# Kernel optimization log

Hardware: AMD Instinct MI355X
Metric: run time of the kernel (lower is better)

Reference implementation:

```python
import jax, jax.numpy as jnp
import numpy as np

B, HOR, E, L = 16, 512, 1024, 12
ACT_NUM, DIM, ADIM = 10, 64, 10
N = 2 * HOR                      # backbone sequence length (test=False)
NPOS = 4 * (1 + HOR)             # wpe table size
D_IN = 3 + DIM * ACT_NUM + ADIM  # embed_transition input dim = 653


def setup_inputs() -> dict:
    key = jax.random.key(0)
    ks = jax.random.split(key, 12)
    s = lambda k, shape: (jax.random.normal(k, shape, jnp.float32) * 0.02)
    return {
        "action_set": jax.random.normal(ks[0], (B, ACT_NUM, DIM), jnp.float32),
        "context_rewards": jax.random.normal(ks[1], (B, HOR, 1), jnp.float32),
        "wpe": s(ks[2], (NPOS, E)),
        "W_emb": s(ks[3], (D_IN, E)),
        "b_emb": jnp.zeros((E,), jnp.float32),
        "Wq": s(ks[4], (L, E, E)),
        "Wk": s(ks[5], (L, E, E)),
        "Wv": s(ks[6], (L, E, E)),
        "ln1_g": jnp.ones((L, E), jnp.float32),
        "ln1_b": jnp.zeros((L, E), jnp.float32),
        "W1": s(ks[7], (L, E, E)),
        "b1": jnp.zeros((L, E), jnp.float32),
        "W2": s(ks[8], (L, E, E)),
        "b2": jnp.zeros((L, E), jnp.float32),
        "ln2_g": jnp.ones((L, E), jnp.float32),
        "ln2_b": jnp.zeros((L, E), jnp.float32),
        "W_pred": s(ks[9], (E, ADIM)),
        "b_pred": jnp.zeros((ADIM,), jnp.float32),
    }


def _layernorm(x, g, b, eps=1e-5):
    mu = x.mean(-1, keepdims=True)
    var = ((x - mu) ** 2).mean(-1, keepdims=True)
    return (x - mu) * jax.lax.rsqrt(var + eps) * g + b


def reference(action_set, context_rewards, wpe, W_emb, b_emb, Wq, Wk, Wv,
              ln1_g, ln1_b, W1, b1, W2, b2, ln2_g, ln2_b, W_pred, b_pred):
    batch = action_set.shape[0]
    hor = context_rewards.shape[1]
    n = 2 * hor
    # --- build interleaved sequence (outer Transformer glue) ---
    a = action_set.reshape(batch, 1, -1)                       # [B,1,DA]
    pair = jnp.concatenate([a, jnp.zeros_like(a)], axis=1)     # [B,2,DA]
    act_set_seq = jnp.tile(pair, (1, hor, 1))                  # [B,2H,DA]
    action_seq = jnp.zeros((batch, n, ADIM + 1), jnp.float32)
    one_seq = jnp.ones((batch, n, 1), jnp.float32)
    pos_seq = jnp.broadcast_to(
        jnp.arange(1, n + 1, dtype=jnp.float32).reshape(1, n, 1), (batch, n, 1))
    seq = jnp.concatenate([act_set_seq, action_seq, one_seq, pos_seq], axis=2)  # [B,N,D_IN]
    # --- DecoderTransformerBackbone ---
    Hs = seq @ W_emb + b_emb
    Hs = Hs + wpe[:n]                                          # positional embedding
    idx = jnp.arange(n)
    # normalized causal mask: row i has 1/(i+1) on j<=i, else 0
    mask = jnp.where(idx[:, None] >= idx[None, :],
                     1.0 / (idx[:, None].astype(jnp.float32) + 1.0), 0.0)
    for l in range(Wq.shape[0]):
        q = Hs @ Wq[l]
        k = Hs @ Wk[l]
        v = Hs @ Wv[l]
        attn = jax.nn.relu(jnp.einsum('bid,bjd->bij', q, k)) * mask
        Hs = Hs + jnp.einsum('bij,bjd->bid', attn, v)
        Hs = _layernorm(Hs, ln1_g[l], ln1_b[l])
        Hs = Hs + (jax.nn.relu(Hs @ W1[l] + b1[l]) @ W2[l] + b2[l])
        Hs = _layernorm(Hs, ln2_g[l], ln2_b[l])
    preds = Hs @ W_pred + b_pred                               # [B,N,ADIM]
    return preds[:, 0::2, :]                                   # [B,HOR,ADIM]
```

## Files before the change

### kernel.cpp

```cpp
#include <hip/hip_runtime.h>
#include <stdint.h>
#include <stddef.h>

#define E_DIM 1024
#define B_SZ  16
#define N_SEQ 1024
#define L_NUM 12
#define ACT_D 640
#define ADIM_ 10

typedef unsigned short u16;
typedef __attribute__((ext_vector_type(8))) short bf16x8;
typedef __attribute__((ext_vector_type(4))) float f32x4;

__device__ __forceinline__ u16 f2bf(float x) {
  union { float f; unsigned int u; } c; c.f = x;
  unsigned int r = c.u + 0x7fffu + ((c.u >> 16) & 1u);
  return (u16)(r >> 16);
}
__device__ __forceinline__ float bf2f(u16 h) {
  union { unsigned int u; float f; } c; c.u = ((unsigned int)h) << 16;
  return c.f;
}

struct us4 { u16 x, y, z, w; };

#define GLD16(gsrc, ldst) __builtin_amdgcn_global_load_lds( \
    (const __attribute__((address_space(1))) void*)(gsrc),  \
    (__attribute__((address_space(3))) void*)(ldst), 16, 0, 0)

#define BM 256
#define BN 128
#define BK 32
#define LDS_A 8192
#define LDS_B 4096
#define BUFU 24576

template<int MODE, int EPI>
__global__ __launch_bounds__(512)
void gemm_nt_mfma(const u16* __restrict__ Ah, const u16* __restrict__ Al,
                  const u16* __restrict__ Bh0, const u16* __restrict__ Bl0,
                  const u16* __restrict__ Bh1, const u16* __restrict__ Bl1,
                  float* __restrict__ Co,
                  u16* __restrict__ Ch0, u16* __restrict__ Cl0,
                  u16* __restrict__ Ch1, u16* __restrict__ Cl1,
                  const float* __restrict__ bias0, const float* __restrict__ bias1,
                  int K, int lda, int ldb, int ldc, int tilesN,
                  long long sA, long long sB, long long sC)
{
  __shared__ u16 smem[3 * BUFU];

  const int tid = threadIdx.x;
  const int bat = blockIdx.y;

  const u16* Bh = Bh0; const u16* Bl = Bl0;
  u16* Ch = Ch0; u16* Cl = Cl0;
  const float* bias = bias0;
  if (blockIdx.z) { Bh = Bh1; Bl = Bl1; Ch = Ch1; Cl = Cl1; bias = bias1; }

  Ah += bat * sA; Al += bat * sA;
  Bh += bat * sB; Bl += bat * sB;

  int bid;
  {
    const int nwg = gridDim.x;
    const int q = nwg >> 3, r = nwg & 7;
    const int xcd = blockIdx.x & 7, off = blockIdx.x >> 3;
    bid = ((xcd < r) ? xcd * (q + 1) : r * (q + 1) + (xcd - r) * q) + off;
  }

  int tm, tn;
  if (MODE == 1) {
    int t = bid, m = 0;
    while ((m + 1) * (m + 2) <= t) m++;
    tm = m; tn = t - m * (m + 1);
  } else {
    tm = bid / tilesN;
    tn = bid % tilesN;
  }
  int kend = K;
  if (MODE == 2) { int c = (tm + 1) * BM; kend = (c < K) ? c : K; }
  const int nk = kend / BK;

  const int ca0 = tid, ca1 = tid + 512, cb0 = tid;
  const int ra0 = ca0 >> 2, ra1 = ca1 >> 2, rb0 = cb0 >> 2;
  const int pa0 = ((ca0 & 3) ^ ((ra0 >> 1) & 3)) * 8;
  const int pa1 = ((ca1 & 3) ^ ((ra1 >> 1) & 3)) * 8;
  const int pb0 = ((cb0 & 3) ^ ((rb0 >> 1) & 3)) * 8;
  const u16* gAh0 = Ah + (long long)(tm * BM + ra0) * lda + pa0;
  const u16* gAh1 = Ah + (long long)(tm * BM + ra1) * lda + pa1;
  const u16* gAl0 = Al + (long long)(tm * BM + ra0) * lda + pa0;
  const u16* gAl1 = Al + (long long)(tm * BM + ra1) * lda + pa1;
  const u16* gBh0 = Bh + (long long)(tn * BN + rb0) * ldb + pb0;
  const u16* gBl0 = Bl + (long long)(tn * BN + rb0) * ldb + pb0;
  const int oa0 = ca0 * 8, oa1 = ca1 * 8, ob0 = cb0 * 8;

  int issued = 0;
  auto stage = [&]() {
    u16* base = smem + (issued % 3) * BUFU;
    GLD16(gAh0, base + oa0);
    GLD16(gAh1, base + oa1);
    GLD16(gAl0, base + LDS_A + oa0);
    GLD16(gAl1, base + LDS_A + oa1);
    GLD16(gBh0, base + 2 * LDS_A + ob0);
    GLD16(gBl0, base + 2 * LDS_A + LDS_B + ob0);
    gAh0 += BK; gAh1 += BK; gAl0 += BK; gAl1 += BK;
    gBh0 += BK; gBl0 += BK;
    issued++;
  };

  const int lane = tid & 63;
  const int w = tid >> 6, wr = w >> 2, wc = w & 3;
  const int fr = lane & 15;
  const int kq = (lane >> 4) * 8;
  const int sa = ((fr >> 1) & 3) << 3;
  const int aoff = ((wr * 128 + fr) * BK + kq) ^ sa;
  const int boff = ((wc * 32 + fr) * BK + kq) ^ sa;

  f32x4 acc[8][2];
  #pragma unroll
  for (int m = 0; m < 8; m++)
    #pragma unroll
    for (int n = 0; n < 2; n++) acc[m][n] = (f32x4){0.f, 0.f, 0.f, 0.f};

  stage(); stage();
  asm volatile("s_waitcnt vmcnt(6)" ::: "memory");
  __builtin_amdgcn_s_barrier();

  for (int t = 0; t < nk; t++) {
    if (issued < nk) stage();
    const u16* sb = smem + (t % 3) * BUFU;

    bf16x8 ah[8], al[8], bh[2], bl[2];
    #pragma unroll
    for (int m = 0; m < 8; m++) ah[m] = *(const bf16x8*)(sb + aoff + m * (16 * BK));
    #pragma unroll
    for (int n = 0; n < 2; n++) bh[n] = *(const bf16x8*)(sb + 2 * LDS_A + boff + n * (16 * BK));
    __builtin_amdgcn_s_setprio(1);
    #pragma unroll
    for (int m = 0; m < 8; m++)
      #pragma unroll
      for (int n = 0; n < 2; n++)
        acc[m][n] = __builtin_amdgcn_mfma_f32_16x16x32_bf16(ah[m], bh[n], acc[m][n], 0, 0, 0);
    __builtin_amdgcn_s_setprio(0);
    #pragma unroll
    for (int n = 0; n < 2; n++) bl[n] = *(const bf16x8*)(sb + 2 * LDS_A + LDS_B + boff + n * (16 * BK));
    __builtin_amdgcn_s_setprio(1);
    #pragma unroll
    for (int m = 0; m < 8; m++)
      #pragma unroll
      for (int n = 0; n < 2; n++)
        acc[m][n] = __builtin_amdgcn_mfma_f32_16x16x32_bf16(ah[m], bl[n], acc[m][n], 0, 0, 0);
    __builtin_amdgcn_s_setprio(0);
    #pragma unroll
    for (int m = 0; m < 8; m++) al[m] = *(const bf16x8*)(sb + LDS_A + aoff + m * (16 * BK));
    __builtin_amdgcn_s_setprio(1);
    #pragma unroll
    for (int m = 0; m < 8; m++)
      #pragma unroll
      for (int n = 0; n < 2; n++)
        acc[m][n] = __builtin_amdgcn_mfma_f32_16x16x32_bf16(al[m], bh[n], acc[m][n], 0, 0, 0);
    __builtin_amdgcn_s_setprio(0);

    if (t + 1 < nk) {
      if (issued > t + 2) asm volatile("s_waitcnt vmcnt(6)" ::: "memory");
      else                asm volatile("s_waitcnt vmcnt(0)" ::: "memory");
      __builtin_amdgcn_s_barrier();
    }
  }

  if (Co) Co += bat * sC;
  if (Ch) { Ch += bat * sC; Cl += bat * sC; }
  #pragma unroll
  for (int m = 0; m < 8; m++) {
    #pragma unroll
    for (int r = 0; r < 4; r++) {
      const long long row = (long long)tm * BM + wr * 128 + m * 16 + (lane >> 4) * 4 + r;
      #pragma unroll
      for (int n = 0; n < 2; n++) {
        const long long col = (long long)tn * BN + wc * 32 + n * 16 + (lane & 15);
        float v = acc[m][n][r];
        if (EPI == 2) { v += bias[col]; v = v > 0.f ? v : 0.f; }
        if (EPI == 4) { v += bias[col]; }
        if (EPI == 3) {
          v = v > 0.f ? v : 0.f;
          v = (col <= row) ? v / (float)(row + 1) : 0.f;
        }
        const long long idx = row * (long long)ldc + col;
        if (EPI == 0 || EPI == 4) {
          Co[idx] = v;
        } else {
          u16 h = f2bf(v);
          Ch[idx] = h;
          Cl[idx] = f2bf(v - bf2f(h));
        }
      }
    }
  }
}

struct TP3 {
  const float* s0; const float* s1; const float* s2;
  u16* h0; u16* l0; u16* h1; u16* l1; u16* h2; u16* l2;
};

__global__ __launch_bounds__(256)
void transpose_split3(TP3 p)
{
  __shared__ float tile[32][33];
  const float* src; u16* dh; u16* dl;
  if (blockIdx.z == 0)      { src = p.s0; dh = p.h0; dl = p.l0; }
  else if (blockIdx.z == 1) { src = p.s1; dh = p.h1; dl = p.l1; }
  else                      { src = p.s2; dh = p.h2; dl = p.l2; }
  const int c0 = blockIdx.x * 32, r0 = blockIdx.y * 32;
  const int tx = threadIdx.x & 31, ty = threadIdx.x >> 5;
  #pragma unroll
  for (int i = ty; i < 32; i += 8)
    tile[i][tx] = src[(long long)(r0 + i) * E_DIM + c0 + tx];
  __syncthreads();
  #pragma unroll
  for (int i = ty; i < 32; i += 8) {
    const float v = tile[tx][i];
    const u16 h = f2bf(v);
    const long long idx = (long long)(c0 + i) * E_DIM + r0 + tx;
    dh[idx] = h;
    dl[idx] = f2bf(v - bf2f(h));
  }
}

__global__ __launch_bounds__(256)
void resid_ln(u16* __restrict__ hh, u16* __restrict__ hl,
              const float* __restrict__ delta,
              const float* __restrict__ g, const float* __restrict__ bta)
{
  __shared__ float red[8];
  const long long row = blockIdx.x;
  u16* hp = hh + row * E_DIM;
  u16* lp = hl + row * E_DIM;
  const float* dp = delta + row * E_DIM;
  const int tid = threadIdx.x;
  const int e = tid * 4;

  us4 hv = *(const us4*)(hp + e);
  us4 lv = *(const us4*)(lp + e);
  float4 d = *(const float4*)(dp + e);
  float x0 = bf2f(hv.x) + bf2f(lv.x) + d.x;
  float x1 = bf2f(hv.y) + bf2f(lv.y) + d.y;
  float x2 = bf2f(hv.z) + bf2f(lv.z) + d.z;
  float x3 = bf2f(hv.w) + bf2f(lv.w) + d.w;
  float s = x0 + x1 + x2 + x3;
  float q = x0 * x0 + x1 * x1 + x2 * x2 + x3 * x3;
  #pragma unroll
  for (int o = 32; o > 0; o >>= 1) { s += __shfl_down(s, o); q += __shfl_down(q, o); }
  const int lane = tid & 63, wv = tid >> 6;
  if (lane == 0) { red[wv] = s; red[wv + 4] = q; }
  __syncthreads();
  const float st = red[0] + red[1] + red[2] + red[3];
  const float qt = red[4] + red[5] + red[6] + red[7];
  const float mu = st * (1.0f / E_DIM);
  const float var = qt * (1.0f / E_DIM) - mu * mu;
  const float rstd = rsqrtf(var + 1e-5f);

  float4 gg = *(const float4*)(g + e);
  float4 bb = *(const float4*)(bta + e);
  float y0 = (x0 - mu) * rstd * gg.x + bb.x;
  float y1 = (x1 - mu) * rstd * gg.y + bb.y;
  float y2 = (x2 - mu) * rstd * gg.z + bb.z;
  float y3 = (x3 - mu) * rstd * gg.w + bb.w;

  us4 ho, lo;
  ho.x = f2bf(y0); lo.x = f2bf(y0 - bf2f(ho.x));
  ho.y = f2bf(y1); lo.y = f2bf(y1 - bf2f(ho.y));
  ho.z = f2bf(y2); lo.z = f2bf(y2 - bf2f(ho.z));
  ho.w = f2bf(y3); lo.w = f2bf(y3 - bf2f(ho.w));
  *(us4*)(hp + e) = ho;
  *(us4*)(lp + e) = lo;
}

__global__ __launch_bounds__(256)
void emb_dot(const float* __restrict__ act, const float* __restrict__ Wemb,
             float* __restrict__ Aemb)
{
  const int e = blockIdx.x * 256 + threadIdx.x;
  const int b = blockIdx.y;
  const float* ab = act + b * ACT_D;
  float s = 0.f;
  for (int d = 0; d < ACT_D; d++)
    s = fmaf(ab[d], Wemb[(long long)d * E_DIM + e], s);
  Aemb[b * E_DIM + e] = s;
}

__global__ __launch_bounds__(256)
void emb_fill(const float* __restrict__ Aemb, const float* __restrict__ Wemb,
              const float* __restrict__ bemb, const float* __restrict__ wpe,
              u16* __restrict__ oh, u16* __restrict__ ol)
{
  const int i = blockIdx.x, b = blockIdx.y;
  const int e = threadIdx.x * 4;
  float4 a;
  if ((i & 1) == 0) a = *(const float4*)(Aemb + b * E_DIM + e);
  else { a.x = 0.f; a.y = 0.f; a.z = 0.f; a.w = 0.f; }
  float4 be = *(const float4*)(bemb + e);
  float4 w1 = *(const float4*)(Wemb + 651LL * E_DIM + e);
  float4 w2 = *(const float4*)(Wemb + 652LL * E_DIM + e);
  float4 pw = *(const float4*)(wpe + (long long)i * E_DIM + e);
  const float pos = (float)(i + 1);
  float y0 = a.x + be.x + w1.x + pos * w2.x + pw.x;
  float y1 = a.y + be.y + w1.y + pos * w2.y + pw.y;
  float y2 = a.z + be.z + w1.z + pos * w2.z + pw.z;
  float y3 = a.w + be.w + w1.w + pos * w2.w + pw.w;
  const long long row = (long long)b * N_SEQ + i;

  us4 ho, lo;
  ho.x = f2bf(y0); lo.x = f2bf(y0 - bf2f(ho.x));
  ho.y = f2bf(y1); lo.y = f2bf(y1 - bf2f(ho.y));
  ho.z = f2bf(y2); lo.z = f2bf(y2 - bf2f(ho.z));
  ho.w = f2bf(y3); lo.w = f2bf(y3 - bf2f(ho.w));
  *(us4*)(oh + row * E_DIM + e) = ho;
  *(us4*)(ol + row * E_DIM + e) = lo;
}

__global__ __launch_bounds__(256)
void pred_k(const u16* __restrict__ hh, const u16* __restrict__ hl,
            const float* __restrict__ Wp, const float* __restrict__ bp,
            float* __restrict__ out)
{
  __shared__ float part[4][ADIM_];
  const int h = blockIdx.x, b = blockIdx.y;
  const long long row = (long long)b * N_SEQ + 2 * h;
  const u16* xh = hh + row * E_DIM;
  const u16* xl = hl + row * E_DIM;
  float acc[ADIM_];
  #pragma unroll
  for (int a = 0; a < ADIM_; a++) acc[a] = 0.f;
  for (int e = threadIdx.x; e < E_DIM; e += 256) {
    const float xv = bf2f(xh[e]) + bf2f(xl[e]);
    const float* wq = Wp + e * ADIM_;
    #pragma unroll
    for (int a = 0; a < ADIM_; a++) acc[a] = fmaf(xv, wq[a], acc[a]);
  }
  const int lane = threadIdx.x & 63, wv = threadIdx.x >> 6;
  #pragma unroll
  for (int a = 0; a < ADIM_; a++)
    #pragma unroll
    for (int o = 32; o > 0; o >>= 1) acc[a] += __shfl_down(acc[a], o);
  if (lane == 0)
    #pragma unroll
    for (int a = 0; a < ADIM_; a++) part[wv][a] = acc[a];
  __syncthreads();
  if (threadIdx.x < ADIM_) {
    const int a = threadIdx.x;
    out[((long long)b * (N_SEQ / 2) + h) * ADIM_ + a] =
        part[0][a] + part[1][a] + part[2][a] + part[3][a] + bp[a];
  }
}

__global__ __launch_bounds__(256)
void fill_sentinel(float* p, int n, float v)
{
  int i = blockIdx.x * 256 + threadIdx.x;
  if (i < n) p[i] = v;
}

extern "C" void kernel_launch(void* const* d_in, const int* in_sizes, int n_in,
                              void* d_out, int out_size, void* d_ws, size_t ws_size,
                              hipStream_t stream)
{
  const float* act  = (const float*)d_in[0];
  const float* wpe  = (const float*)d_in[2];
  const float* Wemb = (const float*)d_in[3];
  const float* bemb = (const float*)d_in[4];
  const float* Wq   = (const float*)d_in[5];
  const float* Wk   = (const float*)d_in[6];
  const float* Wv   = (const float*)d_in[7];
  const float* ln1g = (const float*)d_in[8];
  const float* ln1b = (const float*)d_in[9];
  const float* W1   = (const float*)d_in[10];
  const float* b1   = (const float*)d_in[11];
  const float* W2   = (const float*)d_in[12];
  const float* b2   = (const float*)d_in[13];
  const float* ln2g = (const float*)d_in[14];
  const float* ln2b = (const float*)d_in[15];
  const float* Wp   = (const float*)d_in[16];
  const float* bp   = (const float*)d_in[17];
  float* out = (float*)d_out;

  const long long sQ = (long long)N_SEQ * E_DIM;
  const long long sE = (long long)E_DIM * E_DIM;

  auto need = [&](int G) -> size_t {
    return (size_t)G * sQ * 16 + (size_t)sE * 12
         + (size_t)G * E_DIM * 4 + (size_t)(1 << 20);
  };
  int G = 16;
  while (G > 1 && need(G) > ws_size) G >>= 1;
  if (need(G) > ws_size || d_ws == nullptr || G < 8) {
    fill_sentinel<<<dim3((out_size + 255) / 256), 256, 0, stream>>>(out, out_size, 1.0e7f);
    return;
  }

  char* ws = (char*)d_ws;
  size_t off = 0;
  auto alloc = [&](size_t bytes) -> void* {
    void* p = ws + off;
    off += (bytes + 255) & ~(size_t)255;
    return p;
  };
  u16* hsh = (u16*)alloc((size_t)G * sQ * 2);
  u16* hsl = (u16*)alloc((size_t)G * sQ * 2);
  u16* qh  = (u16*)alloc((size_t)G * sQ * 2);
  u16* ql  = (u16*)alloc((size_t)G * sQ * 2);
  char* kreg = (char*)alloc((size_t)G * sQ * 4);
  u16* kh = (u16*)kreg;
  u16* kl = kh + (size_t)G * sQ;
  float* dbuf = (float*)kreg;
  u16* sh_ = (u16*)alloc((size_t)G * sQ * 2);
  u16* sl_ = (u16*)alloc((size_t)G * sQ * 2);
  u16* wAh = (u16*)alloc((size_t)sE * 2);
  u16* wAl = (u16*)alloc((size_t)sE * 2);
  u16* wBh = (u16*)alloc((size_t)sE * 2);
  u16* wBl = (u16*)alloc((size_t)sE * 2);
  u16* wCh = (u16*)alloc((size_t)sE * 2);
  u16* wCl = (u16*)alloc((size_t)sE * 2);
  float* Aemb = (float*)alloc((size_t)G * E_DIM * 4);

  const int tE = E_DIM / BN;
  const int triS = 20;
  const dim3 gqk((G * N_SEQ / BM) * tE, 1, 2);
  const dim3 gm ((G * N_SEQ / BM) * tE, 1, 1);
  const dim3 gsq(triS, G, 1);
  const dim3 gv ((N_SEQ / BM) * tE, G, 1);

  for (int g0 = 0; g0 < B_SZ; g0 += G) {
    emb_dot<<<dim3(E_DIM / 256, G), 256, 0, stream>>>(act + (long long)g0 * ACT_D, Wemb, Aemb);
    emb_fill<<<dim3(N_SEQ, G), 256, 0, stream>>>(Aemb, Wemb, bemb, wpe, hsh, hsl);

    for (int l = 0; l < L_NUM; l++) {
      const long long wof = (long long)l * sE;
      const long long bof = (long long)l * E_DIM;

      TP3 t2 = {Wq + wof, Wk + wof, Wq + wof, wAh, wAl, wBh, wBl, wAh, wAl};
      transpose_split3<<<dim3(32, 32, 2), 256, 0, stream>>>(t2);
      gemm_nt_mfma<0, 1><<<gqk, 512, 0, stream>>>(hsh, hsl, wAh, wAl, wBh, wBl,
          nullptr, qh, ql, kh, kl, nullptr, nullptr,
          E_DIM, E_DIM, E_DIM, E_DIM, tE, 0, 0, 0);

      TP3 t3 = {Wv + wof, W1 + wof, W2 + wof, wAh, wAl, wBh, wBl, wCh, wCl};
      transpose_split3<<<dim3(32, 32, 3), 256, 0, stream>>>(t3);

      gemm_nt_mfma<1, 3><<<gsq, 512, 0, stream>>>(qh, ql, kh, kl, kh, kl,
          nullptr, sh_, sl_, sh_, sl_, nullptr, nullptr,
          E_DIM, E_DIM, E_DIM, N_SEQ, tE, sQ, sQ, sQ);

      gemm_nt_mfma<0, 1><<<gv, 512, 0, stream>>>(wAh, wAl, hsh, hsl, hsh, hsl,
          nullptr, qh, ql, qh, ql, nullptr, nullptr,
          E_DIM, E_DIM, E_DIM, N_SEQ, tE, 0, sQ, sQ);

      gemm_nt_mfma<2, 0><<<gv, 512, 0, stream>>>(sh_, sl_, qh, ql, qh, ql,
          dbuf, nullptr, nullptr, nullptr, nullptr, nullptr, nullptr,
          N_SEQ, N_SEQ, N_SEQ, E_DIM, tE, sQ, sQ, sQ);

      resid_ln<<<dim3(G * N_SEQ), 256, 0, stream>>>(hsh, hsl, dbuf,
          ln1g + bof, ln1b + bof);

      gemm_nt_mfma<0, 2><<<gm, 512, 0, stream>>>(hsh, hsl, wBh, wBl, wBh, wBl,
          nullptr, qh, ql, qh, ql, b1 + bof, b1 + bof,
          E_DIM, E_DIM, E_DIM, E_DIM, tE, 0, 0, 0);
      gemm_nt_mfma<0, 4><<<gm, 512, 0, stream>>>(qh, ql, wCh, wCl, wCh, wCl,
          dbuf, nullptr, nullptr, nullptr, nullptr, b2 + bof, b2 + bof,
          E_DIM, E_DIM, E_DIM, E_DIM, tE, 0, 0, 0);

      resid_ln<<<dim3(G * N_SEQ), 256, 0, stream>>>(hsh, hsl, dbuf,
          ln2g + bof, ln2b + bof);
    }

    pred_k<<<dim3(N_SEQ / 2, G), 256, 0, stream>>>(hsh, hsl, Wp, bp,
        out + (long long)g0 * (N_SEQ / 2) * ADIM_);
  }
}
```

Before: 9.224 ms.

## Add wide 256-column GEMM tile variant and switch to double-buffered LDS pipeline

Templates the split-bf16 MFMA GEMM on the N tile width, adding a 256x256 tile where each wave computes a 128x64 sub-tile; the 128-wide variant now uses 64x64 wave tiles. The LDS pipeline drops from triple to double buffering, with a full vmcnt(0) wait each iteration. The wide tile is used for QK projection always and for the V, PV and MLP GEMMs when the group size is at least 16. The aim is more operand reuse per LDS load and fewer blocks, at the cost of more accumulator registers, less overlap of global loads with compute, and fewer workgroups to fill the CUs.

```diff
diff --git a/kernel.cpp b/kernel.cpp
--- a/kernel.cpp
+++ b/kernel.cpp
@@ -30,13 +30,9 @@
     (__attribute__((address_space(3))) void*)(ldst), 16, 0, 0)
 
 #define BM 256
-#define BN 128
 #define BK 32
-#define LDS_A 8192
-#define LDS_B 4096
-#define BUFU 24576
-
-template<int MODE, int EPI>
+
+template<int MODE, int EPI, int BNT>
 __global__ __launch_bounds__(512)
 void gemm_nt_mfma(const u16* __restrict__ Ah, const u16* __restrict__ Al,
                   const u16* __restrict__ Bh0, const u16* __restrict__ Bl0,
@@ -48,7 +44,14 @@
                   int K, int lda, int ldb, int ldc, int tilesN,
                   long long sA, long long sB, long long sC)
 {
-  __shared__ u16 smem[3 * BUFU];
+  constexpr int LA = BM * BK;
+  constexpr int LB = BNT * BK;
+  constexpr int BUFU = 2 * LA + 2 * LB;
+  __shared__ u16 smem[2 * BUFU];
+
+  constexpr int WAVE_R = (BNT == 256) ? 128 : 64;
+  constexpr int WGC = BNT / 64;
+  constexpr int MA = WAVE_R / 16;
 
   const int tid = threadIdx.x;
   const int bat = blockIdx.y;
@@ -82,89 +85,98 @@
   if (MODE == 2) { int c = (tm + 1) * BM; kend = (c < K) ? c : K; }
   const int nk = kend / BK;
 
-  const int ca0 = tid, ca1 = tid + 512, cb0 = tid;
-  const int ra0 = ca0 >> 2, ra1 = ca1 >> 2, rb0 = cb0 >> 2;
+  const int ca0 = tid, ca1 = tid + 512;
+  const int ra0 = ca0 >> 2, ra1 = ca1 >> 2;
   const int pa0 = ((ca0 & 3) ^ ((ra0 >> 1) & 3)) * 8;
   const int pa1 = ((ca1 & 3) ^ ((ra1 >> 1) & 3)) * 8;
+  const int cb0 = tid, cb1 = tid + 512;
+  const int rb0 = cb0 >> 2, rb1 = cb1 >> 2;
   const int pb0 = ((cb0 & 3) ^ ((rb0 >> 1) & 3)) * 8;
+  const int pb1 = ((cb1 & 3) ^ ((rb1 >> 1) & 3)) * 8;
+
   const u16* gAh0 = Ah + (long long)(tm * BM + ra0) * lda + pa0;
   const u16* gAh1 = Ah + (long long)(tm * BM + ra1) * lda + pa1;
   const u16* gAl0 = Al + (long long)(tm * BM + ra0) * lda + pa0;
   const u16* gAl1 = Al + (long long)(tm * BM + ra1) * lda + pa1;
-  const u16* gBh0 = Bh + (long long)(tn * BN + rb0) * ldb + pb0;
-  const u16* gBl0 = Bl + (long long)(tn * BN + rb0) * ldb + pb0;
-  const int oa0 = ca0 * 8, oa1 = ca1 * 8, ob0 = cb0 * 8;
-
-  int issued = 0;
-  auto stage = [&]() {
-    u16* base = smem + (issued % 3) * BUFU;
+  const u16* gBh0 = Bh + (long long)(tn * BNT + rb0) * ldb + pb0;
+  const u16* gBl0 = Bl + (long long)(tn * BNT + rb0) * ldb + pb0;
+  const u16* gBh1 = Bh + (long long)(tn * BNT + rb1) * ldb + pb1;
+  const u16* gBl1 = Bl + (long long)(tn * BNT + rb1) * ldb + pb1;
+  const int oa0 = ca0 * 8, oa1 = ca1 * 8, ob0 = cb0 * 8, ob1 = cb1 * 8;
+
+  auto stage = [&](int buf) {
+    u16* base = smem + buf * BUFU;
     GLD16(gAh0, base + oa0);
     GLD16(gAh1, base + oa1);
-    GLD16(gAl0, base + LDS_A + oa0);
-    GLD16(gAl1, base + LDS_A + oa1);
-    GLD16(gBh0, base + 2 * LDS_A + ob0);
-    GLD16(gBl0, base + 2 * LDS_A + LDS_B + ob0);
+    GLD16(gAl0, base + LA + oa0);
+    GLD16(gAl1, base + LA + oa1);
+    GLD16(gBh0, base + 2 * LA + ob0);
+    GLD16(gBl0, base + 2 * LA + LB + ob0);
+    if (BNT == 256) {
+      GLD16(gBh1, base + 2 * LA + ob1);
+      GLD16(gBl1, base + 2 * LA + LB + ob1);
+    }
     gAh0 += BK; gAh1 += BK; gAl0 += BK; gAl1 += BK;
     gBh0 += BK; gBl0 += BK;
-    issued++;
+    if (BNT == 256) { gBh1 += BK; gBl1 += BK; }
   };
 
   const int lane = tid & 63;
-  const int w = tid >> 6, wr = w >> 2, wc = w & 3;
+  const int w = tid >> 6;
+  const int wr = w / WGC, wc = w % WGC;
   const int fr = lane & 15;
   const int kq = (lane >> 4) * 8;
   const int sa = ((fr >> 1) & 3) << 3;
-  const int aoff = ((wr * 128 + fr) * BK + kq) ^ sa;
-  const int boff = ((wc * 32 + fr) * BK + kq) ^ sa;
-
-  f32x4 acc[8][2];
-  #pragma unroll
-  for (int m = 0; m < 8; m++)
-    #pragma unroll
-    for (int n = 0; n < 2; n++) acc[m][n] = (f32x4){0.f, 0.f, 0.f, 0.f};
-
-  stage(); stage();
-  asm volatile("s_waitcnt vmcnt(6)" ::: "memory");
+  const int aoff = ((wr * WAVE_R + fr) * BK + kq) ^ sa;
+  const int boff = ((wc * 64 + fr) * BK + kq) ^ sa;
+
+  f32x4 acc[MA][4];
+  #pragma unroll
+  for (int m = 0; m < MA; m++)
+    #pragma unroll
+    for (int n = 0; n < 4; n++) acc[m][n] = (f32x4){0.f, 0.f, 0.f, 0.f};
+
+  stage(0);
+  asm volatile("s_waitcnt vmcnt(0)" ::: "memory");
   __builtin_amdgcn_s_barrier();
 
   for (int t = 0; t < nk; t++) {
-    if (issued < nk) stage();
-    const u16* sb = smem + (t % 3) * BUFU;
-
-    bf16x8 ah[8], al[8], bh[2], bl[2];
-    #pragma unroll
-    for (int m = 0; m < 8; m++) ah[m] = *(const bf16x8*)(sb + aoff + m * (16 * BK));
-    #pragma unroll
-    for (int n = 0; n < 2; n++) bh[n] = *(const bf16x8*)(sb + 2 * LDS_A + boff + n * (16 * BK));
+    if (t + 1 < nk) stage((t + 1) & 1);
+    const u16* sb = smem + (t & 1) * BUFU;
+
+    bf16x8 ah[MA], al[MA], bh[4], bl[4];
+    #pragma unroll
+    for (int m = 0; m < MA; m++) ah[m] = *(const bf16x8*)(sb + aoff + m * (16 * BK));
+    #pragma unroll
+    for (int n = 0; n < 4; n++) bh[n] = *(const bf16x8*)(sb + 2 * LA + boff + n * (16 * BK));
     __builtin_amdgcn_s_setprio(1);
     #pragma unroll
-    for (int m = 0; m < 8; m++)
+    for (int m = 0; m < MA; m++)
       #pragma unroll
-      for (int n = 0; n < 2; n++)
+      for (int n = 0; n < 4; n++)
         acc[m][n] = __builtin_amdgcn_mfma_f32_16x16x32_bf16(ah[m], bh[n], acc[m][n], 0, 0, 0);
     __builtin_amdgcn_s_setprio(0);
     #pragma unroll
-    for (int n = 0; n < 2; n++) bl[n] = *(const bf16x8*)(sb + 2 * LDS_A + LDS_B + boff + n * (16 * BK));
+    for (int m = 0; m < MA; m++) al[m] = *(const bf16x8*)(sb + LA + aoff + m * (16 * BK));
     __builtin_amdgcn_s_setprio(1);
     #pragma unroll
-    for (int m = 0; m < 8; m++)
+    for (int m = 0; m < MA; m++)
       #pragma unroll
-      for (int n = 0; n < 2; n++)
+      for (int n = 0; n < 4; n++)
+        acc[m][n] = __builtin_amdgcn_mfma_f32_16x16x32_bf16(al[m], bh[n], acc[m][n], 0, 0, 0);
+    __builtin_amdgcn_s_setprio(0);
+    #pragma unroll
+    for (int n = 0; n < 4; n++) bl[n] = *(const bf16x8*)(sb + 2 * LA + LB + boff + n * (16 * BK));
+    __builtin_amdgcn_s_setprio(1);
+    #pragma unroll
+    for (int m = 0; m < MA; m++)
+      #pragma unroll
+      for (int n = 0; n < 4; n++)
         acc[m][n] = __builtin_amdgcn_mfma_f32_16x16x32_bf16(ah[m], bl[n], acc[m][n], 0, 0, 0);
     __builtin_amdgcn_s_setprio(0);
-    #pragma unroll
-    for (int m = 0; m < 8; m++) al[m] = *(const bf16x8*)(sb + LDS_A + aoff + m * (16 * BK));
-    __builtin_amdgcn_s_setprio(1);
-    #pragma unroll
-    for (int m = 0; m < 8; m++)
-      #pragma unroll
-      for (int n = 0; n < 2; n++)
-        acc[m][n] = __builtin_amdgcn_mfma_f32_16x16x32_bf16(al[m], bh[n], acc[m][n], 0, 0, 0);
-    __builtin_amdgcn_s_setprio(0);
 
     if (t + 1 < nk) {
-      if (issued > t + 2) asm volatile("s_waitcnt vmcnt(6)" ::: "memory");
-      else                asm volatile("s_waitcnt vmcnt(0)" ::: "memory");
+      asm volatile("s_waitcnt vmcnt(0)" ::: "memory");
       __builtin_amdgcn_s_barrier();
     }
   }
@@ -172,13 +184,13 @@
   if (Co) Co += bat * sC;
   if (Ch) { Ch += bat * sC; Cl += bat * sC; }
   #pragma unroll
-  for (int m = 0; m < 8; m++) {
+  for (int m = 0; m < MA; m++) {
     #pragma unroll
     for (int r = 0; r < 4; r++) {
-      const long long row = (long long)tm * BM + wr * 128 + m * 16 + (lane >> 4) * 4 + r;
+      const long long row = (long long)tm * BM + wr * WAVE_R + m * 16 + (lane >> 4) * 4 + r;
       #pragma unroll
-      for (int n = 0; n < 2; n++) {
-        const long long col = (long long)tn * BN + wc * 32 + n * 16 + (lane & 15);
+      for (int n = 0; n < 4; n++) {
+        const long long col = (long long)tn * BNT + wc * 64 + n * 16 + (lane & 15);
         float v = acc[m][n][r];
         if (EPI == 2) { v += bias[col]; v = v > 0.f ? v : 0.f; }
         if (EPI == 4) { v += bias[col]; }
@@ -424,12 +436,15 @@
   u16* wCl = (u16*)alloc((size_t)sE * 2);
   float* Aemb = (float*)alloc((size_t)G * E_DIM * 4);
 
-  const int tE = E_DIM / BN;
+  const bool wide = (G >= 16);
   const int triS = 20;
-  const dim3 gqk((G * N_SEQ / BM) * tE, 1, 2);
-  const dim3 gm ((G * N_SEQ / BM) * tE, 1, 1);
+
+  const dim3 gqk((G * N_SEQ / BM) * (E_DIM / 256), 1, 2);
   const dim3 gsq(triS, G, 1);
-  const dim3 gv ((N_SEQ / BM) * tE, G, 1);
+  const dim3 gm256((G * N_SEQ / BM) * (E_DIM / 256), 1, 1);
+  const dim3 gm128((G * N_SEQ / BM) * (E_DIM / 128), 1, 1);
+  const dim3 gv256((N_SEQ / BM) * (E_DIM / 256), G, 1);
+  const dim3 gv128((N_SEQ / BM) * (E_DIM / 128), G, 1);
 
   for (int g0 = 0; g0 < B_SZ; g0 += G) {
     emb_dot<<<dim3(E_DIM / 256, G), 256, 0, stream>>>(act + (long long)g0 * ACT_D, Wemb, Aemb);
@@ -441,34 +456,54 @@
 
       TP3 t2 = {Wq + wof, Wk + wof, Wq + wof, wAh, wAl, wBh, wBl, wAh, wAl};
       transpose_split3<<<dim3(32, 32, 2), 256, 0, stream>>>(t2);
-      gemm_nt_mfma<0, 1><<<gqk, 512, 0, stream>>>(hsh, hsl, wAh, wAl, wBh, wBl,
+      gemm_nt_mfma<0, 1, 256><<<gqk, 512, 0, stream>>>(hsh, hsl, wAh, wAl, wBh, wBl,
           nullptr, qh, ql, kh, kl, nullptr, nullptr,
-          E_DIM, E_DIM, E_DIM, E_DIM, tE, 0, 0, 0);
+          E_DIM, E_DIM, E_DIM, E_DIM, E_DIM / 256, 0, 0, 0);
 
       TP3 t3 = {Wv + wof, W1 + wof, W2 + wof, wAh, wAl, wBh, wBl, wCh, wCl};
       transpose_split3<<<dim3(32, 32, 3), 256, 0, stream>>>(t3);
 
-      gemm_nt_mfma<1, 3><<<gsq, 512, 0, stream>>>(qh, ql, kh, kl, kh, kl,
+      gemm_nt_mfma<1, 3, 128><<<gsq, 512, 0, stream>>>(qh, ql, kh, kl, kh, kl,
           nullptr, sh_, sl_, sh_, sl_, nullptr, nullptr,
-          E_DIM, E_DIM, E_DIM, N_SEQ, tE, sQ, sQ, sQ);
-
-      gemm_nt_mfma<0, 1><<<gv, 512, 0, stream>>>(wAh, wAl, hsh, hsl, hsh, hsl,
-          nullptr, qh, ql, qh, ql, nullptr, nullptr,
-          E_DIM, E_DIM, E_DIM, N_SEQ, tE, 0, sQ, sQ);
-
-      gemm_nt_mfma<2, 0><<<gv, 512, 0, stream>>>(sh_, sl_, qh, ql, qh, ql,
-          dbuf, nullptr, nullptr, nullptr, nullptr, nullptr, nullptr,
-          N_SEQ, N_SEQ, N_SEQ, E_DIM, tE, sQ, sQ, sQ);
+          E_DIM, E_DIM, E_DIM, N_SEQ, 0, sQ, sQ, sQ);
+
+      if (wide)
+        gemm_nt_mfma<0, 1, 256><<<gv256, 512, 0, stream>>>(wAh, wAl, hsh, hsl, hsh, hsl,
+            nullptr, qh, ql, qh, ql, nullptr, nullptr,
+            E_DIM, E_DIM, E_DIM, N_SEQ, E_DIM / 256, 0, sQ, sQ);
+      else
+        gemm_nt_mfma<0, 1, 128><<<gv128, 512, 0, stream>>>(wAh, wAl, hsh, hsl, hsh, hsl,
+            nullptr, qh, ql, qh, ql, nullptr, nullptr,
+            E_DIM, E_DIM, E_DIM, N_SEQ, E_DIM / 128, 0, sQ, sQ);
+
+      if (wide)
+        gemm_nt_mfma<2, 0, 256><<<gv256, 512, 0, stream>>>(sh_, sl_, qh, ql, qh, ql,
+            dbuf, nullptr, nullptr, nullptr, nullptr, nullptr, nullptr,
+            N_SEQ, N_SEQ, N_SEQ, E_DIM, E_DIM / 256, sQ, sQ, sQ);
+      else
+        gemm_nt_mfma<2, 0, 128><<<gv128, 512, 0, stream>>>(sh_, sl_, qh, ql, qh, ql,
+            dbuf, nullptr, nullptr, nullptr, nullptr, nullptr, nullptr,
+            N_SEQ, N_SEQ, N_SEQ, E_DIM, E_DIM / 128, sQ, sQ, sQ);
 
       resid_ln<<<dim3(G * N_SEQ), 256, 0, stream>>>(hsh, hsl, dbuf,
           ln1g + bof, ln1b + bof);
 
-      gemm_nt_mfma<0, 2><<<gm, 512, 0, stream>>>(hsh, hsl, wBh, wBl, wBh, wBl,
-          nullptr, qh, ql, qh, ql, b1 + bof, b1 + bof,
-          E_DIM, E_DIM, E_DIM, E_DIM, tE, 0, 0, 0);
-      gemm_nt_mfma<0, 4><<<gm, 512, 0, stream>>>(qh, ql, wCh, wCl, wCh, wCl,
-          dbuf, nullptr, nullptr, nullptr, nullptr, b2 + bof, b2 + bof,
-          E_DIM, E_DIM, E_DIM, E_DIM, tE, 0, 0, 0);
+      if (wide)
+        gemm_nt_mfma<0, 2, 256><<<gm256, 512, 0, stream>>>(hsh, hsl, wBh, wBl, wBh, wBl,
+            nullptr, qh, ql, qh, ql, b1 + bof, b1 + bof,
+            E_DIM, E_DIM, E_DIM, E_DIM, E_DIM / 256, 0, 0, 0);
+      else
+        gemm_nt_mfma<0, 2, 128><<<gm128, 512, 0, stream>>>(hsh, hsl, wBh, wBl, wBh, wBl,
+            nullptr, qh, ql, qh, ql, b1 + bof, b1 + bof,
+            E_DIM, E_DIM, E_DIM, E_DIM, E_DIM / 128, 0, 0, 0);
+      if (wide)
+        gemm_nt_mfma<0, 4, 256><<<gm256, 512, 0, stream>>>(qh, ql, wCh, wCl, wCh, wCl,
+            dbuf, nullptr, nullptr, nullptr, nullptr, b2 + bof, b2 + bof,
+            E_DIM, E_DIM, E_DIM, E_DIM, E_DIM / 256, 0, 0, 0);
+      else
+        gemm_nt_mfma<0, 4, 128><<<gm128, 512, 0, stream>>>(qh, ql, wCh, wCl, wCh, wCl,
+            dbuf, nullptr, nullptr, nullptr, nullptr, b2 + bof, b2 + bof,
+            E_DIM, E_DIM, E_DIM, E_DIM, E_DIM / 128, 0, 0, 0);
 
       resid_ln<<<dim3(G * N_SEQ), 256, 0, stream>>>(hsh, hsl, dbuf,
           ln2g + bof, ln2b + bof);
```

Result: faster. 8.890 ms (-3.6%).
